# Optimization experiments

Measured on AMD Instinct MI355X. Metric: run time of the kernel, lower is better.

The kernel has to match this reference:

```python
import jax, jax.numpy as jnp
import numpy as np

B, NOBJ, MLEN, D, H = 32, 256, 256, 1024, 16
DK = D // H
NEG = -1e9


def setup_inputs() -> dict:
    key = jax.random.key(0)
    ks = jax.random.split(key, 16)

    def lin(kw, kb, fin, fout):
        s = 1.0 / np.sqrt(fin)
        w = jax.random.uniform(kw, (fin, fout), jnp.float32, -s, s)
        b = jax.random.uniform(kb, (fout,), jnp.float32, -s, s)
        return w, b

    v = jax.random.normal(ks[0], (B, NOBJ, D), jnp.float32)
    q = jax.random.normal(ks[1], (B, MLEN, D), jnp.float32)
    v_mask = jax.random.randint(ks[2], (B, NOBJ), 0, 2).astype(jnp.float32)
    q_mask = jax.random.randint(ks[3], (B, MLEN), 0, 2).astype(jnp.float32)
    # guarantee at least one valid position per row (avoid 0/0 in masked mean)
    v_mask = v_mask.at[:, 0].set(1.0)
    q_mask = q_mask.at[:, 0].set(1.0)

    w_v4q, b_v4q = lin(ks[4], ks[5], D, D)
    w_q4v, b_q4v = lin(ks[6], ks[7], D, D)
    w_vlin, b_vlin = lin(ks[8], ks[9], D, 3 * D)
    w_qlin, b_qlin = lin(ks[10], ks[11], D, 3 * D)
    w_vout, b_vout = lin(ks[12], ks[13], D, D)
    w_qout, b_qout = lin(ks[14], ks[15], D, D)

    return dict(v=v, q=q, v_mask=v_mask, q_mask=q_mask,
                w_v4q=w_v4q, b_v4q=b_v4q, w_q4v=w_q4v, b_q4v=b_q4v,
                w_vlin=w_vlin, b_vlin=b_vlin, w_qlin=w_qlin, b_qlin=b_qlin,
                w_vout=w_vout, b_vout=b_vout, w_qout=w_qout, b_qout=b_qout)


def _attend(qh, kh, vh, mask):
    # qh,kh,vh: [B,N,D]; mask: [B,N]
    b, n, _ = qh.shape
    qh = qh.reshape(b, n, H, DK)
    kh = kh.reshape(b, n, H, DK)
    vh = vh.reshape(b, n, H, DK)
    scores = jnp.einsum('bqhd,bkhd->bhqk', qh, kh)
    # faithful to torch: masked_fill(-1e9) THEN divide by sqrt(dk)
    scores = jnp.where(mask[:, None, None, :] == 0, NEG, scores) / np.sqrt(DK)
    attn = jax.nn.softmax(scores, axis=-1)
    out = jnp.einsum('bhqk,bkhd->bqhd', attn, vh)
    return out.reshape(b, n, H * DK)


def reference(v, q, v_mask, q_mask,
              w_v4q, b_v4q, w_q4v, b_q4v,
              w_vlin, b_vlin, w_qlin, b_qlin,
              w_vout, b_vout, w_qout, b_qout):
    v_mean = (v * v_mask[:, :, None]).sum(1) / v_mask.sum(1, keepdims=True)
    q_mean = (q * q_mask[:, :, None]).sum(1) / q_mask.sum(1, keepdims=True)
    v4q_gate = jax.nn.sigmoid(jax.nn.relu(v_mean) @ w_v4q + b_v4q)[:, None, :]
    q4v_gate = jax.nn.sigmoid(jax.nn.relu(q_mean) @ w_q4v + b_q4v)[:, None, :]

    v_trans = (jax.nn.relu(v) @ w_vlin + b_vlin) * v_mask[:, :, None]
    q_trans = (jax.nn.relu(q) @ w_qlin + b_qlin) * q_mask[:, :, None]
    v_k, v_q, v_v = jnp.split(v_trans, 3, axis=2)
    q_k, q_q, q_v = jnp.split(q_trans, 3, axis=2)

    v_update = _attend((1 + q4v_gate) * v_q, (1 + q4v_gate) * v_k, v_v, v_mask)
    q_update = _attend((1 + v4q_gate) * q_q, (1 + v4q_gate) * q_k, q_v, q_mask)

    updated_v = (v + v_update) @ w_vout + b_vout
    updated_q = (q + q_update) @ w_qout + b_qout
    return updated_v, updated_q
```

## Files before the change

kernel.cpp:

```cpp
#include <hip/hip_runtime.h>
#include <cstdint>

typedef unsigned short u16;
typedef __attribute__((ext_vector_type(8))) short s16x8;
typedef __attribute__((ext_vector_type(4))) float f32x4;

__device__ __forceinline__ u16 f2bf(float f) {
  unsigned int u = __float_as_uint(f);
  return (u16)((u + 0x7FFFu + ((u >> 16) & 1u)) >> 16);
}
__device__ __forceinline__ float bf2f(u16 b) {
  return __uint_as_float(((unsigned int)b) << 16);
}
__device__ __forceinline__ f32x4 mfma16(s16x8 a, s16x8 b, f32x4 c) {
  return __builtin_amdgcn_mfma_f32_16x16x32_bf16(a, b, c, 0, 0, 0);
}
__device__ __forceinline__ void gload16(const void* g, void* l) {
  __builtin_amdgcn_global_load_lds((const __attribute__((address_space(1))) void*)g,
                                   (__attribute__((address_space(3))) void*)l, 16, 0, 0);
}

__global__ __launch_bounds__(256) void k_wt(const float* __restrict__ in0, u16* __restrict__ out0,
                                            const float* __restrict__ in1, u16* __restrict__ out1,
                                            int K, int N) {
  const float* in = blockIdx.z ? in1 : in0;
  u16* out = blockIdx.z ? out1 : out0;
  __shared__ float tile[32][33];
  int n0 = blockIdx.x * 32, k0 = blockIdx.y * 32;
  int tx = threadIdx.x & 31, ty = threadIdx.x >> 5;
#pragma unroll
  for (int i = 0; i < 32; i += 8)
    tile[ty + i][tx] = in[(size_t)(k0 + ty + i) * N + n0 + tx];
  __syncthreads();
#pragma unroll
  for (int i = 0; i < 32; i += 8)
    out[(size_t)(n0 + ty + i) * K + k0 + tx] = f2bf(tile[tx][ty + i]);
}

__global__ __launch_bounds__(256) void k_prep(const float* __restrict__ v,
                                              const float* __restrict__ q,
                                              const float* __restrict__ vm,
                                              const float* __restrict__ qm,
                                              u16* __restrict__ rbf,
                                              float* __restrict__ raw,
                                              float* __restrict__ msum) {
  int b = blockIdx.x;
  int mod = blockIdx.y & 1, dc = blockIdx.y >> 1;
  int ns = blockIdx.z;
  const float* x = mod ? q : v;
  const float* mk = (mod ? qm : vm) + b * 256;
  int d = dc * 256 + threadIdx.x;
  const float* xb = x + ((size_t)b * 256 + ns * 32) * 1024 + d;
  u16* ob = rbf + ((size_t)(mod * 8192 + b * 256 + ns * 32)) * 1024 + d;
  float s = 0.f;
#pragma unroll 4
  for (int n = 0; n < 32; ++n) {
    float xv = xb[(size_t)n * 1024];
    s = fmaf(xv, mk[ns * 32 + n], s);
    ob[(size_t)n * 1024] = f2bf(xv > 0.f ? xv : 0.f);
  }
  atomicAdd(&raw[(mod * 32 + b) * 1024 + d], s);
  if (threadIdx.x == 0 && dc == 0) {
    float t = 0.f;
    for (int n = 0; n < 32; ++n) t += mk[ns * 32 + n];
    atomicAdd(&msum[mod * 32 + b], t);
  }
}

__global__ __launch_bounds__(256) void k_gate(const float* __restrict__ raw,
                                              const float* __restrict__ msum,
                                              const float* __restrict__ Wq4v,
                                              const float* __restrict__ bq4v,
                                              const float* __restrict__ Wv4q,
                                              const float* __restrict__ bv4q,
                                              float* __restrict__ gsv,
                                              float* __restrict__ gsq) {
  int b = blockIdx.y, z = blockIdx.z;
  int srcmod = z == 0 ? 1 : 0;
  const float* W = z == 0 ? Wq4v : Wv4q;
  const float* bias = z == 0 ? bq4v : bv4q;
  float* gs = z == 0 ? gsv : gsq;
  const float* r = raw + (srcmod * 32 + b) * 1024;
  float inv = 1.f / msum[srcmod * 32 + b];
  int d = blockIdx.x * 256 + threadIdx.x;
  float acc = bias[d];
#pragma unroll 8
  for (int k = 0; k < 1024; ++k) {
    float m = r[k] * inv;
    m = m > 0.f ? m : 0.f;
    acc = fmaf(m, W[(size_t)k * 1024 + d], acc);
  }
  gs[b * 1024 + d] = 1.f + 1.f / (1.f + expf(-acc));
}

template <int EPI>
__global__ __launch_bounds__(512, 2) void k_mm(const u16* __restrict__ A,
                                               const u16* __restrict__ BTv,
                                               const u16* __restrict__ BTq,
                                               const float* __restrict__ biasv,
                                               const float* __restrict__ biasq,
                                               u16* __restrict__ outv_b,
                                               u16* __restrict__ outq_b,
                                               float* __restrict__ outf,
                                               const float* __restrict__ maskv,
                                               const float* __restrict__ maskq,
                                               const float* __restrict__ gsv,
                                               const float* __restrict__ gsq) {
  __shared__ u16 lA[4][8192];
  __shared__ u16 lB[4][8192];
  constexpr int NU = 32;
  int nwg = gridDim.x, cpx = nwg >> 3, bid = blockIdx.x;
  int id = (bid & 7) * cpx + (bid >> 3);
  int by = id & 63, bx = id >> 6;
  int m0 = by * 256, n0 = bx * 256;
  int half = (m0 >= 8192);
  const u16* BT = half ? BTq : BTv;

  int tid = threadIdx.x, w = tid >> 6, lane = tid & 63;
  int wr = w >> 2, wc = w & 3;
  int la = lane & 15, lb = lane >> 4;

  const char* srcA[2]; const char* srcB[2]; int dstO[2];
#pragma unroll
  for (int s = 0; s < 2; ++s) {
    int o = s * 8192 + tid * 16;
    int row = o >> 6, colb = o & 63;
    int sw = (row & 3) << 4;
    srcA[s] = (const char*)A + (size_t)(m0 + row) * 2048 + (colb ^ sw);
    srcB[s] = (const char*)BT + (size_t)(n0 + row) * 2048 + (colb ^ sw);
    dstO[s] = o;
  }
  int aoffs[8], boffs[4];
#pragma unroll
  for (int i = 0; i < 8; ++i) {
    int r = wr * 128 + i * 16 + la;
    aoffs[i] = r * 64 + ((lb * 16) ^ ((r & 3) << 4));
  }
#pragma unroll
  for (int j = 0; j < 4; ++j) {
    int r = wc * 64 + j * 16 + la;
    boffs[j] = r * 64 + ((lb * 16) ^ ((r & 3) << 4));
  }

  f32x4 acc[8][4] = {};

#pragma unroll
  for (int s = 0; s < 2; ++s) gload16(srcA[s], (char*)&lA[0][0] + dstO[s]);
#pragma unroll
  for (int s = 0; s < 2; ++s) gload16(srcB[s], (char*)&lB[0][0] + dstO[s]);
#pragma unroll
  for (int s = 0; s < 2; ++s) gload16(srcA[s] + 64, (char*)&lA[1][0] + dstO[s]);
#pragma unroll
  for (int s = 0; s < 2; ++s) gload16(srcB[s] + 64, (char*)&lB[1][0] + dstO[s]);
  asm volatile("s_waitcnt vmcnt(4)" ::: "memory");
  __builtin_amdgcn_s_barrier();

  for (int u = 0; u < NU; ++u) {
    const char* cA = (const char*)&lA[u & 3][0];
    const char* cB = (const char*)&lB[u & 3][0];
    int pu = u + 2;
    char* wA = (char*)&lA[pu & 3][0];
    char* wB = (char*)&lB[pu & 3][0];
    bool pf = pu < NU;
    s16x8 a0[4], b0[4];
#pragma unroll
    for (int j = 0; j < 4; ++j) b0[j] = *(const s16x8*)(cB + boffs[j]);
#pragma unroll
    for (int i = 0; i < 4; ++i) a0[i] = *(const s16x8*)(cA + aoffs[i]);
    if (pf) {
      gload16(srcA[0] + pu * 64, wA + dstO[0]);
      gload16(srcA[1] + pu * 64, wA + dstO[1]);
    }
    __builtin_amdgcn_s_barrier();
    asm volatile("s_waitcnt lgkmcnt(0)" ::: "memory");
    __builtin_amdgcn_sched_barrier(0);
    __builtin_amdgcn_s_setprio(1);
#pragma unroll
    for (int i = 0; i < 4; ++i)
#pragma unroll
      for (int j = 0; j < 4; ++j)
        acc[i][j] = mfma16(a0[i], b0[j], acc[i][j]);
    __builtin_amdgcn_s_setprio(0);
    __builtin_amdgcn_s_barrier();
    s16x8 a1[4];
#pragma unroll
    for (int i = 0; i < 4; ++i) a1[i] = *(const s16x8*)(cA + aoffs[4 + i]);
    if (pf) {
      gload16(srcB[0] + pu * 64, wB + dstO[0]);
      gload16(srcB[1] + pu * 64, wB + dstO[1]);
    }
    __builtin_amdgcn_s_barrier();
    asm volatile("s_waitcnt lgkmcnt(0)" ::: "memory");
    __builtin_amdgcn_sched_barrier(0);
    __builtin_amdgcn_s_setprio(1);
#pragma unroll
    for (int i = 0; i < 4; ++i)
#pragma unroll
      for (int j = 0; j < 4; ++j)
        acc[4 + i][j] = mfma16(a1[i], b0[j], acc[4 + i][j]);
    __builtin_amdgcn_s_setprio(0);
    if (u < NU - 2) asm volatile("s_waitcnt vmcnt(4)" ::: "memory");
    else            asm volatile("s_waitcnt vmcnt(0)" ::: "memory");
    __builtin_amdgcn_s_barrier();
  }

  const float* bias = half ? biasq : biasv;
  const float* mask = half ? maskq : maskv;
  const float* gs = half ? gsq : gsv;
#pragma unroll
  for (int i = 0; i < 8; ++i) {
    int mbase = m0 + wr * 128 + i * 16 + lb * 4;
#pragma unroll
    for (int j = 0; j < 4; ++j) {
      int n = n0 + wc * 64 + j * 16 + la;
      float bn = bias[n];
#pragma unroll
      for (int r = 0; r < 4; ++r) {
        int m = mbase + r;
        float val = acc[i][j][r] + bn;
        if (EPI == 0) {
          int mloc = m & 8191;
          val *= mask[mloc];
          if (n < 2048) val *= gs[((mloc >> 8) << 10) + (n & 1023)];
          (half ? outq_b : outv_b)[(size_t)mloc * 3072 + n] = f2bf(val);
        } else {
          outf[(size_t)m * 1024 + n] = val;
        }
      }
    }
  }
}

__global__ __launch_bounds__(256) void k_vtrans(const u16* __restrict__ tr0,
                                                const u16* __restrict__ tr1,
                                                u16* __restrict__ vt0,
                                                u16* __restrict__ vt1) {
  int bz = blockIdx.z;
  int mod = bz >> 5, b = bz & 31;
  const u16* tr = mod ? tr1 : tr0;
  u16* vt = mod ? vt1 : vt0;
  __shared__ u16 tile[64 * 64];
  int kt = blockIdx.x, dt = blockIdx.y;
  int t = threadIdx.x, tx = t & 7, ty = t >> 3;
  const u16* src = tr + (size_t)b * 786432 + 2048 + dt * 64;
#pragma unroll
  for (int i = 0; i < 2; ++i) {
    int key = ty + i * 32;
    s16x8 vv = *(const s16x8*)(src + (size_t)(kt * 64 + key) * 3072 + tx * 8);
    int oct = key >> 3;
#pragma unroll
    for (int j = 0; j < 8; ++j) {
      int d = tx * 8 + j;
      tile[d * 64 + ((oct ^ (d >> 3)) << 3) + (key & 7)] = (u16)vv[j];
    }
  }
  __syncthreads();
  u16* dst = vt + (size_t)b * 262144 + (size_t)dt * 64 * 256 + kt * 64;
#pragma unroll
  for (int i = 0; i < 2; ++i) {
    int d = ty + i * 32;
    s16x8 ov = *(const s16x8*)&tile[d * 64 + ((tx ^ (d >> 3)) << 3)];
    *(s16x8*)(dst + (size_t)d * 256 + tx * 8) = ov;
  }
}

__global__ __launch_bounds__(256) void k_attn(const u16* __restrict__ tr0,
                                              const u16* __restrict__ tr1,
                                              const u16* __restrict__ vt0,
                                              const u16* __restrict__ vt1,
                                              const float* __restrict__ mk0,
                                              const float* __restrict__ mk1,
                                              const float* __restrict__ x0,
                                              const float* __restrict__ x1,
                                              u16* __restrict__ ao0,
                                              u16* __restrict__ ao1) {
  int z = blockIdx.z;
  const u16* trans = z ? tr1 : tr0;
  const u16* vt = z ? vt1 : vt0;
  const float* mask = z ? mk1 : mk0;
  const float* xorig = z ? x1 : x0;
  u16* attin = z ? ao1 : ao0;

  __shared__ u16 Kl[16384];
  __shared__ u16 Vt[64 * 256];
  int h = blockIdx.x >> 2, qc = blockIdx.x & 3;
  int b = blockIdx.y;
  int t = threadIdx.x, w = t >> 6, lane = t & 63;
  const u16* tb = trans + (size_t)b * 256 * 3072;
  const char* tbc = (const char*)tb;

#pragma unroll
  for (int i = 0; i < 8; ++i) {
    int o = i * 4096 + t * 16;
    int row = o >> 7, colb = o & 127;
    gload16(tbc + (size_t)row * 6144 + h * 128 + (colb ^ ((row & 7) << 4)),
            (char*)Kl + o);
  }
  const char* vtb = (const char*)(vt + (size_t)b * 262144 + (size_t)h * 64 * 256);
#pragma unroll
  for (int i = 0; i < 8; ++i) {
    int o = i * 4096 + t * 16;
    int d = o >> 9, oct = (o >> 4) & 31;
    gload16(vtb + d * 512 + ((oct ^ (d & 7)) << 4), (char*)Vt + o);
  }
  __syncthreads();

  int la = lane & 15, lb = lane >> 4;
  int q0 = qc * 64 + w * 16;
  const u16* qrow = tb + (size_t)(q0 + la) * 3072 + 1024 + h * 64;
  s16x8 qf0 = *(const s16x8*)(qrow + lb * 8);
  s16x8 qf1 = *(const s16x8*)(qrow + 32 + lb * 8);

  f32x4 sc[16];
#pragma unroll
  for (int nt = 0; nt < 16; ++nt) {
    int row = nt * 16 + la;
    int sw = (row & 7) << 4;
    s16x8 kf0 = *(const s16x8*)((const char*)Kl + row * 128 + ((lb * 16) ^ sw));
    s16x8 kf1 = *(const s16x8*)((const char*)Kl + row * 128 + ((64 + lb * 16) ^ sw));
    f32x4 s = {0.f, 0.f, 0.f, 0.f};
    s = mfma16(qf0, kf0, s);
    s = mfma16(qf1, kf1, s);
    sc[nt] = s;
  }
  __syncthreads();

  u16* Pw = Kl + w * 4096;
  const float* mb = mask + b * 256;
  float rsum[4] = {0.f, 0.f, 0.f, 0.f};
#pragma unroll
  for (int nt = 0; nt < 16; ++nt) {
    int key = nt * 16 + la;
    float km = mb[key];
    int quad = key >> 3, klow = key & 7;
#pragma unroll
    for (int r = 0; r < 4; ++r) {
      float p = (km != 0.f) ? expf(sc[nt][r] * 0.125f) : 0.f;
      u16 pb = f2bf(p);
      int lr = lb * 4 + r;
      rsum[r] += bf2f(pb);
      Pw[lr * 256 + ((quad ^ (lr & 7)) << 3) + klow] = pb;
    }
  }
#pragma unroll
  for (int r = 0; r < 4; ++r) {
    rsum[r] += __shfl_xor(rsum[r], 1);
    rsum[r] += __shfl_xor(rsum[r], 2);
    rsum[r] += __shfl_xor(rsum[r], 4);
    rsum[r] += __shfl_xor(rsum[r], 8);
  }
  __syncthreads();

  f32x4 o[4] = {};
  for (int kt = 0; kt < 8; ++kt) {
    int pq = kt * 4 + lb;
    s16x8 pa = *(const s16x8*)&Pw[la * 256 + ((pq ^ (la & 7)) << 3)];
#pragma unroll
    for (int dt = 0; dt < 4; ++dt) {
      int d = dt * 16 + la;
      s16x8 vb = *(const s16x8*)&Vt[d * 256 + ((pq ^ (d & 7)) << 3)];
      o[dt] = mfma16(pa, vb, o[dt]);
    }
  }

#pragma unroll
  for (int dt = 0; dt < 4; ++dt) {
    int dcol = h * 64 + dt * 16 + la;
#pragma unroll
    for (int r = 0; r < 4; ++r) {
      int qr = q0 + lb * 4 + r;
      size_t gi = ((size_t)b * 256 + qr) * 1024 + dcol;
      attin[gi] = f2bf(xorig[gi] + o[dt][r] / rsum[r]);
    }
  }
}

extern "C" void kernel_launch(void* const* d_in, const int* in_sizes, int n_in,
                              void* d_out, int out_size, void* d_ws, size_t ws_size,
                              hipStream_t stream) {
  const float* v      = (const float*)d_in[0];
  const float* q      = (const float*)d_in[1];
  const float* v_mask = (const float*)d_in[2];
  const float* q_mask = (const float*)d_in[3];
  const float* w_v4q  = (const float*)d_in[4];
  const float* b_v4q  = (const float*)d_in[5];
  const float* w_q4v  = (const float*)d_in[6];
  const float* b_q4v  = (const float*)d_in[7];
  const float* w_vlin = (const float*)d_in[8];
  const float* b_vlin = (const float*)d_in[9];
  const float* w_qlin = (const float*)d_in[10];
  const float* b_qlin = (const float*)d_in[11];
  const float* w_vout = (const float*)d_in[12];
  const float* b_vout = (const float*)d_in[13];
  const float* w_qout = (const float*)d_in[14];
  const float* b_qout = (const float*)d_in[15];
  float* out = (float*)d_out;

  char* ws = (char*)d_ws;
  u16* rbf       = (u16*)(ws);
  u16* rbf_v     = rbf;
  u16* rbf_q     = (u16*)(ws + 16777216);
  u16* woutT_v   = (u16*)(ws + 33554432);
  u16* woutT_q   = (u16*)(ws + 35651584);
  u16* trans_v   = (u16*)(ws + 37748736);
  u16* wlinT_v   = (u16*)(ws + 88080384);
  u16* wlinT_q   = (u16*)(ws + 94371840);
  float* raw     = (float*)(ws + 100663296);
  float* msum    = (float*)(ws + 100925440);
  float* gs_v    = (float*)(ws + 100925696);
  float* gs_q    = (float*)(ws + 101056768);
  u16* vT_v      = (u16*)(ws + 88080384);
  u16* trans_q   = (u16*)d_out;
  u16* vT_q      = (u16*)((char*)d_out + 50331648);

  dim3 blk(256);
  hipMemsetAsync(raw, 0, 262400, stream);
  k_wt<<<dim3(96, 32, 2), blk, 0, stream>>>(w_vlin, wlinT_v, w_qlin, wlinT_q, 1024, 3072);
  k_wt<<<dim3(32, 32, 2), blk, 0, stream>>>(w_vout, woutT_v, w_qout, woutT_q, 1024, 1024);
  k_prep<<<dim3(32, 8, 8), blk, 0, stream>>>(v, q, v_mask, q_mask, rbf, raw, msum);
  k_gate<<<dim3(4, 32, 2), blk, 0, stream>>>(raw, msum, w_q4v, b_q4v, w_v4q, b_v4q, gs_v, gs_q);
  k_mm<0><<<dim3(768), dim3(512), 0, stream>>>(rbf, wlinT_v, wlinT_q, b_vlin, b_qlin,
                                               trans_v, trans_q, nullptr,
                                               v_mask, q_mask, gs_v, gs_q);
  k_vtrans<<<dim3(4, 16, 64), blk, 0, stream>>>(trans_v, trans_q, vT_v, vT_q);
  k_attn<<<dim3(64, 32, 2), blk, 0, stream>>>(trans_v, trans_q, vT_v, vT_q,
                                              v_mask, q_mask, v, q, rbf_v, rbf_q);
  k_mm<1><<<dim3(256), dim3(512), 0, stream>>>(rbf, woutT_v, woutT_q, b_vout, b_qout,
                                               nullptr, nullptr, out,
                                               nullptr, nullptr, nullptr, nullptr);
}
```

Baseline: 546.3 us.

## Restructure GEMM main loop into finer-grained staged pipeline with new LDS swizzle

Rewrites the k_mm main loop so each K-step loads all eight A fragments and then two B fragments at a time, splitting the MFMA work into four quarter-phases, each gated by barriers. Global-to-LDS prefetches are interleaved one per phase across a four-slot ring that is kept three to four half-steps ahead. The LDS XOR swizzle changes from row&3 to (row>>1)&3 to reduce bank conflicts for the new read pattern. The aim is better overlap of memory traffic with MFMA and fewer LDS conflicts. In exchange there are more barriers per iteration and more register pressure from holding eight A fragments.

After: 536.8 us. About the same (-1.7%).

```diff
diff --git a/kernel.cpp b/kernel.cpp
--- a/kernel.cpp
+++ b/kernel.cpp
@@ -108,7 +108,6 @@
                                                const float* __restrict__ gsq) {
   __shared__ u16 lA[4][8192];
   __shared__ u16 lB[4][8192];
-  constexpr int NU = 32;
   int nwg = gridDim.x, cpx = nwg >> 3, bid = blockIdx.x;
   int id = (bid & 7) * cpx + (bid >> 3);
   int by = id & 63, bx = id >> 6;
@@ -120,87 +119,114 @@
   int wr = w >> 2, wc = w & 3;
   int la = lane & 15, lb = lane >> 4;
 
-  const char* srcA[2]; const char* srcB[2]; int dstO[2];
-#pragma unroll
-  for (int s = 0; s < 2; ++s) {
-    int o = s * 8192 + tid * 16;
-    int row = o >> 6, colb = o & 63;
-    int sw = (row & 3) << 4;
-    srcA[s] = (const char*)A + (size_t)(m0 + row) * 2048 + (colb ^ sw);
-    srcB[s] = (const char*)BT + (size_t)(n0 + row) * 2048 + (colb ^ sw);
-    dstO[s] = o;
-  }
+  int o0 = tid * 16, o1 = 8192 + tid * 16;
+  int r0 = o0 >> 6, c0 = o0 & 63;
+  int r1 = o1 >> 6, c1 = o1 & 63;
+  const char* sA0 = (const char*)A + (size_t)(m0 + r0) * 2048 + (c0 ^ (((r0 >> 1) & 3) << 4));
+  const char* sA1 = (const char*)A + (size_t)(m0 + r1) * 2048 + (c1 ^ (((r1 >> 1) & 3) << 4));
+  const char* sB0 = (const char*)BT + (size_t)(n0 + r0) * 2048 + (c0 ^ (((r0 >> 1) & 3) << 4));
+  const char* sB1 = (const char*)BT + (size_t)(n0 + r1) * 2048 + (c1 ^ (((r1 >> 1) & 3) << 4));
+
+  auto stA = [&](int slot, int kt, int kh) {
+    int go = kt * 128 + kh * 64;
+    gload16(sA0 + go, (char*)&lA[slot][0] + o0);
+    gload16(sA1 + go, (char*)&lA[slot][0] + o1);
+  };
+  auto stB = [&](int slot, int kt, int kh) {
+    int go = kt * 128 + kh * 64;
+    gload16(sB0 + go, (char*)&lB[slot][0] + o0);
+    gload16(sB1 + go, (char*)&lB[slot][0] + o1);
+  };
+
   int aoffs[8], boffs[4];
 #pragma unroll
   for (int i = 0; i < 8; ++i) {
     int r = wr * 128 + i * 16 + la;
-    aoffs[i] = r * 64 + ((lb * 16) ^ ((r & 3) << 4));
+    aoffs[i] = r * 64 + ((lb * 16) ^ (((r >> 1) & 3) << 4));
   }
 #pragma unroll
   for (int j = 0; j < 4; ++j) {
     int r = wc * 64 + j * 16 + la;
-    boffs[j] = r * 64 + ((lb * 16) ^ ((r & 3) << 4));
+    boffs[j] = r * 64 + ((lb * 16) ^ (((r >> 1) & 3) << 4));
   }
 
   f32x4 acc[8][4] = {};
-
-#pragma unroll
-  for (int s = 0; s < 2; ++s) gload16(srcA[s], (char*)&lA[0][0] + dstO[s]);
-#pragma unroll
-  for (int s = 0; s < 2; ++s) gload16(srcB[s], (char*)&lB[0][0] + dstO[s]);
-#pragma unroll
-  for (int s = 0; s < 2; ++s) gload16(srcA[s] + 64, (char*)&lA[1][0] + dstO[s]);
-#pragma unroll
-  for (int s = 0; s < 2; ++s) gload16(srcB[s] + 64, (char*)&lB[1][0] + dstO[s]);
-  asm volatile("s_waitcnt vmcnt(4)" ::: "memory");
-  __builtin_amdgcn_s_barrier();
-
-  for (int u = 0; u < NU; ++u) {
-    const char* cA = (const char*)&lA[u & 3][0];
-    const char* cB = (const char*)&lB[u & 3][0];
-    int pu = u + 2;
-    char* wA = (char*)&lA[pu & 3][0];
-    char* wB = (char*)&lB[pu & 3][0];
-    bool pf = pu < NU;
-    s16x8 a0[4], b0[4];
-#pragma unroll
-    for (int j = 0; j < 4; ++j) b0[j] = *(const s16x8*)(cB + boffs[j]);
-#pragma unroll
-    for (int i = 0; i < 4; ++i) a0[i] = *(const s16x8*)(cA + aoffs[i]);
-    if (pf) {
-      gload16(srcA[0] + pu * 64, wA + dstO[0]);
-      gload16(srcA[1] + pu * 64, wA + dstO[1]);
-    }
+  s16x8 a[8], b[2];
+
+  auto rdA8 = [&](int slot) {
+#pragma unroll
+    for (int i = 0; i < 8; ++i)
+      a[i] = *(const s16x8*)((const char*)&lA[slot][0] + aoffs[i]);
+  };
+  auto rdB2 = [&](int slot, int jh) {
+    b[0] = *(const s16x8*)((const char*)&lB[slot][0] + boffs[jh * 2]);
+    b[1] = *(const s16x8*)((const char*)&lB[slot][0] + boffs[jh * 2 + 1]);
+  };
+  auto gate = [&]() {
     __builtin_amdgcn_s_barrier();
     asm volatile("s_waitcnt lgkmcnt(0)" ::: "memory");
     __builtin_amdgcn_sched_barrier(0);
     __builtin_amdgcn_s_setprio(1);
-#pragma unroll
-    for (int i = 0; i < 4; ++i)
-#pragma unroll
-      for (int j = 0; j < 4; ++j)
-        acc[i][j] = mfma16(a0[i], b0[j], acc[i][j]);
+  };
+  auto mfJ0 = [&]() {
+#pragma unroll
+    for (int i = 0; i < 8; ++i) {
+      acc[i][0] = mfma16(a[i], b[0], acc[i][0]);
+      acc[i][1] = mfma16(a[i], b[1], acc[i][1]);
+    }
+  };
+  auto mfJ1 = [&]() {
+#pragma unroll
+    for (int i = 0; i < 8; ++i) {
+      acc[i][2] = mfma16(a[i], b[0], acc[i][2]);
+      acc[i][3] = mfma16(a[i], b[1], acc[i][3]);
+    }
+  };
+  auto close = [&]() {
     __builtin_amdgcn_s_setprio(0);
     __builtin_amdgcn_s_barrier();
-    s16x8 a1[4];
-#pragma unroll
-    for (int i = 0; i < 4; ++i) a1[i] = *(const s16x8*)(cA + aoffs[4 + i]);
-    if (pf) {
-      gload16(srcB[0] + pu * 64, wB + dstO[0]);
-      gload16(srcB[1] + pu * 64, wB + dstO[1]);
-    }
+  };
+
+  stA(0, 0, 0); stB(0, 0, 0); stA(1, 0, 1); stB(1, 0, 1);
+  stA(2, 1, 0); stB(2, 1, 0); stA(3, 1, 1);
+  asm volatile("s_waitcnt vmcnt(6)" ::: "memory");
+  __builtin_amdgcn_s_barrier();
+
+#pragma unroll 1
+  for (int it = 0; it < 8; ++it) {
+    int k1t = 2 * it + 1, nx = 2 * it + 2, nx2 = 2 * it + 3;
+    bool pf = it < 7;
+    rdA8(0); rdB2(0, 0);
+    stB(3, k1t, 1);
+    gate(); mfJ0(); close();
+    rdB2(0, 1);
+    if (pf) stA(0, nx, 0);
+    gate(); mfJ1(); close();
+    rdA8(1); rdB2(1, 0);
+    if (pf) stB(0, nx, 0);
+    gate(); mfJ0(); close();
+    rdB2(1, 1);
+    if (pf) stA(1, nx, 1);
+    gate(); mfJ1();
+    __builtin_amdgcn_s_setprio(0);
+    if (pf) asm volatile("s_waitcnt vmcnt(6)" ::: "memory");
+    else    asm volatile("s_waitcnt vmcnt(0)" ::: "memory");
     __builtin_amdgcn_s_barrier();
-    asm volatile("s_waitcnt lgkmcnt(0)" ::: "memory");
-    __builtin_amdgcn_sched_barrier(0);
-    __builtin_amdgcn_s_setprio(1);
-#pragma unroll
-    for (int i = 0; i < 4; ++i)
-#pragma unroll
-      for (int j = 0; j < 4; ++j)
-        acc[4 + i][j] = mfma16(a1[i], b0[j], acc[4 + i][j]);
+    rdA8(2); rdB2(2, 0);
+    if (pf) stB(1, nx, 1);
+    gate(); mfJ0(); close();
+    rdB2(2, 1);
+    if (pf) stA(2, nx2, 0);
+    gate(); mfJ1(); close();
+    rdA8(3); rdB2(3, 0);
+    if (pf) stB(2, nx2, 0);
+    gate(); mfJ0(); close();
+    rdB2(3, 1);
+    if (pf) stA(3, nx2, 1);
+    gate(); mfJ1();
     __builtin_amdgcn_s_setprio(0);
-    if (u < NU - 2) asm volatile("s_waitcnt vmcnt(4)" ::: "memory");
-    else            asm volatile("s_waitcnt vmcnt(0)" ::: "memory");
+    if (pf) asm volatile("s_waitcnt vmcnt(6)" ::: "memory");
+    else    asm volatile("s_waitcnt vmcnt(0)" ::: "memory");
     __builtin_amdgcn_s_barrier();
   }
 
```

## Shrink GEMM tiles to 128x128 with 4 waves and double buffering

Applied to the files above, without the earlier changes.

Rewrites the bf16 GEMM kernel from 256x256 tiles with 8 waves and a 4-stage LDS ring to 128x128 tiles with 4 waves and a simple 2-stage double buffer. The LDS swizzle also changes. The grid grows from 768/256 to 3072/1024 blocks, which is meant to improve occupancy and load balance across CUs. In exchange each tile has lower arithmetic intensity, so more global traffic, and the pipeline is shallower because it waits on vmcnt(0) every iteration.

After: 555.1 us. No clear change (+1.6%).

```diff
diff --git a/kernel.cpp b/kernel.cpp
--- a/kernel.cpp
+++ b/kernel.cpp
@@ -94,7 +94,7 @@
 }
 
 template <int EPI>
-__global__ __launch_bounds__(512, 2) void k_mm(const u16* __restrict__ A,
+__global__ __launch_bounds__(256, 4) void k_mm(const u16* __restrict__ A,
                                                const u16* __restrict__ BTv,
                                                const u16* __restrict__ BTq,
                                                const float* __restrict__ biasv,
@@ -106,72 +106,65 @@
                                                const float* __restrict__ maskq,
                                                const float* __restrict__ gsv,
                                                const float* __restrict__ gsq) {
-  __shared__ u16 lA[4][8192];
-  __shared__ u16 lB[4][8192];
-  constexpr int NU = 32;
+  __shared__ __align__(16) u16 lA[2][4096];
+  __shared__ __align__(16) u16 lB[2][4096];
   int nwg = gridDim.x, cpx = nwg >> 3, bid = blockIdx.x;
   int id = (bid & 7) * cpx + (bid >> 3);
-  int by = id & 63, bx = id >> 6;
-  int m0 = by * 256, n0 = bx * 256;
+  int by = id & 127, bx = id >> 7;
+  int m0 = by * 128, n0 = bx * 128;
   int half = (m0 >= 8192);
   const u16* BT = half ? BTq : BTv;
 
   int tid = threadIdx.x, w = tid >> 6, lane = tid & 63;
-  int wr = w >> 2, wc = w & 3;
+  int wr = w >> 1, wc = w & 1;
   int la = lane & 15, lb = lane >> 4;
 
-  const char* srcA[2]; const char* srcB[2]; int dstO[2];
-#pragma unroll
-  for (int s = 0; s < 2; ++s) {
-    int o = s * 8192 + tid * 16;
-    int row = o >> 6, colb = o & 63;
-    int sw = (row & 3) << 4;
-    srcA[s] = (const char*)A + (size_t)(m0 + row) * 2048 + (colb ^ sw);
-    srcB[s] = (const char*)BT + (size_t)(n0 + row) * 2048 + (colb ^ sw);
-    dstO[s] = o;
-  }
-  int aoffs[8], boffs[4];
-#pragma unroll
-  for (int i = 0; i < 8; ++i) {
-    int r = wr * 128 + i * 16 + la;
-    aoffs[i] = r * 64 + ((lb * 16) ^ ((r & 3) << 4));
+  int o0 = tid * 16, o1 = 4096 + tid * 16;
+  int r0 = o0 >> 6, c0 = o0 & 63;
+  int r1 = o1 >> 6, c1 = o1 & 63;
+  const char* sA0 = (const char*)A + (size_t)(m0 + r0) * 2048 + (c0 ^ (((r0 >> 1) & 3) << 4));
+  const char* sA1 = (const char*)A + (size_t)(m0 + r1) * 2048 + (c1 ^ (((r1 >> 1) & 3) << 4));
+  const char* sB0 = (const char*)BT + (size_t)(n0 + r0) * 2048 + (c0 ^ (((r0 >> 1) & 3) << 4));
+  const char* sB1 = (const char*)BT + (size_t)(n0 + r1) * 2048 + (c1 ^ (((r1 >> 1) & 3) << 4));
+
+  int aoffs[4], boffs[4];
+#pragma unroll
+  for (int i = 0; i < 4; ++i) {
+    int r = wr * 64 + i * 16 + la;
+    aoffs[i] = r * 64 + ((lb * 16) ^ (((r >> 1) & 3) << 4));
   }
 #pragma unroll
   for (int j = 0; j < 4; ++j) {
     int r = wc * 64 + j * 16 + la;
-    boffs[j] = r * 64 + ((lb * 16) ^ ((r & 3) << 4));
-  }
-
-  f32x4 acc[8][4] = {};
-
-#pragma unroll
-  for (int s = 0; s < 2; ++s) gload16(srcA[s], (char*)&lA[0][0] + dstO[s]);
-#pragma unroll
-  for (int s = 0; s < 2; ++s) gload16(srcB[s], (char*)&lB[0][0] + dstO[s]);
-#pragma unroll
-  for (int s = 0; s < 2; ++s) gload16(srcA[s] + 64, (char*)&lA[1][0] + dstO[s]);
-#pragma unroll
-  for (int s = 0; s < 2; ++s) gload16(srcB[s] + 64, (char*)&lB[1][0] + dstO[s]);
-  asm volatile("s_waitcnt vmcnt(4)" ::: "memory");
+    boffs[j] = r * 64 + ((lb * 16) ^ (((r >> 1) & 3) << 4));
+  }
+
+  f32x4 acc[4][4] = {};
+
+  gload16(sA0, (char*)&lA[0][0] + o0);
+  gload16(sA1, (char*)&lA[0][0] + o1);
+  gload16(sB0, (char*)&lB[0][0] + o0);
+  gload16(sB1, (char*)&lB[0][0] + o1);
+  asm volatile("s_waitcnt vmcnt(0)" ::: "memory");
   __builtin_amdgcn_s_barrier();
 
-  for (int u = 0; u < NU; ++u) {
-    const char* cA = (const char*)&lA[u & 3][0];
-    const char* cB = (const char*)&lB[u & 3][0];
-    int pu = u + 2;
-    char* wA = (char*)&lA[pu & 3][0];
-    char* wB = (char*)&lB[pu & 3][0];
-    bool pf = pu < NU;
-    s16x8 a0[4], b0[4];
-#pragma unroll
-    for (int j = 0; j < 4; ++j) b0[j] = *(const s16x8*)(cB + boffs[j]);
-#pragma unroll
-    for (int i = 0; i < 4; ++i) a0[i] = *(const s16x8*)(cA + aoffs[i]);
-    if (pf) {
-      gload16(srcA[0] + pu * 64, wA + dstO[0]);
-      gload16(srcA[1] + pu * 64, wA + dstO[1]);
-    }
-    __builtin_amdgcn_s_barrier();
+#pragma unroll 1
+  for (int t = 0; t < 32; ++t) {
+    int cur = t & 1, nxt = cur ^ 1;
+    if (t + 1 < 32) {
+      int go = (t + 1) * 64;
+      gload16(sA0 + go, (char*)&lA[nxt][0] + o0);
+      gload16(sA1 + go, (char*)&lA[nxt][0] + o1);
+      gload16(sB0 + go, (char*)&lB[nxt][0] + o0);
+      gload16(sB1 + go, (char*)&lB[nxt][0] + o1);
+    }
+    s16x8 a[4], b[4];
+#pragma unroll
+    for (int i = 0; i < 4; ++i)
+      a[i] = *(const s16x8*)((const char*)&lA[cur][0] + aoffs[i]);
+#pragma unroll
+    for (int j = 0; j < 4; ++j)
+      b[j] = *(const s16x8*)((const char*)&lB[cur][0] + boffs[j]);
     asm volatile("s_waitcnt lgkmcnt(0)" ::: "memory");
     __builtin_amdgcn_sched_barrier(0);
     __builtin_amdgcn_s_setprio(1);
@@ -179,28 +172,9 @@
     for (int i = 0; i < 4; ++i)
 #pragma unroll
       for (int j = 0; j < 4; ++j)
-        acc[i][j] = mfma16(a0[i], b0[j], acc[i][j]);
+        acc[i][j] = mfma16(a[i], b[j], acc[i][j]);
     __builtin_amdgcn_s_setprio(0);
-    __builtin_amdgcn_s_barrier();
-    s16x8 a1[4];
-#pragma unroll
-    for (int i = 0; i < 4; ++i) a1[i] = *(const s16x8*)(cA + aoffs[4 + i]);
-    if (pf) {
-      gload16(srcB[0] + pu * 64, wB + dstO[0]);
-      gload16(srcB[1] + pu * 64, wB + dstO[1]);
-    }
-    __builtin_amdgcn_s_barrier();
-    asm volatile("s_waitcnt lgkmcnt(0)" ::: "memory");
-    __builtin_amdgcn_sched_barrier(0);
-    __builtin_amdgcn_s_setprio(1);
-#pragma unroll
-    for (int i = 0; i < 4; ++i)
-#pragma unroll
-      for (int j = 0; j < 4; ++j)
-        acc[4 + i][j] = mfma16(a1[i], b0[j], acc[4 + i][j]);
-    __builtin_amdgcn_s_setprio(0);
-    if (u < NU - 2) asm volatile("s_waitcnt vmcnt(4)" ::: "memory");
-    else            asm volatile("s_waitcnt vmcnt(0)" ::: "memory");
+    asm volatile("s_waitcnt vmcnt(0)" ::: "memory");
     __builtin_amdgcn_s_barrier();
   }
 
@@ -208,8 +182,8 @@
   const float* mask = half ? maskq : maskv;
   const float* gs = half ? gsq : gsv;
 #pragma unroll
-  for (int i = 0; i < 8; ++i) {
-    int mbase = m0 + wr * 128 + i * 16 + lb * 4;
+  for (int i = 0; i < 4; ++i) {
+    int mbase = m0 + wr * 64 + i * 16 + lb * 4;
 #pragma unroll
     for (int j = 0; j < 4; ++j) {
       int n = n0 + wc * 64 + j * 16 + la;
@@ -419,13 +393,13 @@
   k_wt<<<dim3(32, 32, 2), blk, 0, stream>>>(w_vout, woutT_v, w_qout, woutT_q, 1024, 1024);
   k_prep<<<dim3(32, 8, 8), blk, 0, stream>>>(v, q, v_mask, q_mask, rbf, raw, msum);
   k_gate<<<dim3(4, 32, 2), blk, 0, stream>>>(raw, msum, w_q4v, b_q4v, w_v4q, b_v4q, gs_v, gs_q);
-  k_mm<0><<<dim3(768), dim3(512), 0, stream>>>(rbf, wlinT_v, wlinT_q, b_vlin, b_qlin,
-                                               trans_v, trans_q, nullptr,
-                                               v_mask, q_mask, gs_v, gs_q);
+  k_mm<0><<<dim3(3072), blk, 0, stream>>>(rbf, wlinT_v, wlinT_q, b_vlin, b_qlin,
+                                          trans_v, trans_q, nullptr,
+                                          v_mask, q_mask, gs_v, gs_q);
   k_vtrans<<<dim3(4, 16, 64), blk, 0, stream>>>(trans_v, trans_q, vT_v, vT_q);
   k_attn<<<dim3(64, 32, 2), blk, 0, stream>>>(trans_v, trans_q, vT_v, vT_q,
                                               v_mask, q_mask, v, q, rbf_v, rbf_q);
-  k_mm<1><<<dim3(256), dim3(512), 0, stream>>>(rbf, woutT_v, woutT_q, b_vout, b_qout,
-                                               nullptr, nullptr, out,
-                                               nullptr, nullptr, nullptr, nullptr);
-}
+  k_mm<1><<<dim3(1024), blk, 0, stream>>>(rbf, woutT_v, woutT_q, b_vout, b_qout,
+                                          nullptr, nullptr, out,
+                                          nullptr, nullptr, nullptr, nullptr);
+}
```
